# Performance work log

Measured on AMD Instinct MI355X. Metric: run time of the kernel, lower is better.

## Reference

```python
import jax, jax.numpy as jnp
import numpy as np

NEG = -1e9  # additive mask value


def _longformer_attn(x, kv_mask, Wq, bq, Wk, bk, Wv, bv, Wqg, bqg, Wkg, bkg, Wvg, bvg, Wo, bo, H, w, G):
    # x: [B, S, E]; kv_mask: [B, S] (mask*-1 > 0 => global; first G tokens are global by construction)
    B, S, E = x.shape
    D = E // H
    scale = 1.0 / float(D) ** 0.5

    def proj(W, b):  # -> [B, H, S, D]
        return (x @ W + b).reshape(B, S, H, D).transpose(0, 2, 1, 3)

    q = proj(Wq, bq) * scale
    k = proj(Wk, bk)
    v = proj(Wv, bv)

    nc = S // w  # number of query chunks of size w
    # banded keys/values: each chunk of w queries sees a 3w key band (prev/cur/next chunk)
    idx = (jnp.arange(nc) * w)[:, None] + jnp.arange(3 * w)[None, :]  # [nc, 3w] into padded seq

    def band(t):  # [B,H,S,D] -> [B,H,nc,3w,D]
        tp = jnp.pad(t, ((0, 0), (0, 0), (w, w), (0, 0)))
        return tp[:, :, idx, :]

    k3, v3 = band(k), band(v)
    qc = q.reshape(B, H, nc, w, D)
    s_win = jnp.einsum('bhcwd,bhced->bhcwe', qc, k3)  # [B,H,nc,w,3w]

    i = jnp.arange(w)[:, None]
    j = jnp.arange(3 * w)[None, :]
    rel_ok = (j >= i) & (j <= i + 2 * w)  # |key_pos - query_pos| <= w
    keypos = (jnp.arange(nc) * w)[:, None, None] + (jnp.arange(3 * w) - w)[None, None, :]  # [nc,1,3w]
    ok = rel_ok[None] & (keypos >= 0) & (keypos < S) & (keypos >= G)  # global keys handled separately
    s_win = jnp.where(ok[None, None], s_win, NEG)

    # every query also attends to the G global keys (standard projections)
    s_g = jnp.einsum('bhqd,bhgd->bhqg', q, k[:, :, :G])  # [B,H,S,G]
    s_all = jnp.concatenate([s_g, s_win.reshape(B, H, S, 3 * w)], axis=-1)
    p = jax.nn.softmax(s_all, axis=-1)  # joint softmax over global + window keys
    p_g, p_w = p[..., :G], p[..., G:].reshape(B, H, nc, w, 3 * w)

    out = jnp.einsum('bhcwe,bhced->bhcwd', p_w, v3).reshape(B, H, S, D)
    out = out + jnp.einsum('bhqg,bhgd->bhqd', p_g, v[:, :, :G])

    # global query rows: full attention over all tokens with the *global* projections
    qg = (x @ Wqg + bqg).reshape(B, S, H, D).transpose(0, 2, 1, 3)[:, :, :G] * scale
    kg = (x @ Wkg + bkg).reshape(B, S, H, D).transpose(0, 2, 1, 3)
    vg = (x @ Wvg + bvg).reshape(B, S, H, D).transpose(0, 2, 1, 3)
    pg = jax.nn.softmax(jnp.einsum('bhgd,bhsd->bhgs', qg, kg), axis=-1)  # [B,H,G,S]
    out = out.at[:, :, :G].set(jnp.einsum('bhgs,bhsd->bhgd', pg, vg))

    ctx = out.transpose(0, 2, 1, 3).reshape(B, S, E)
    return ctx @ Wo + bo  # wrapper's self.output Linear


def setup_inputs() -> dict:
    key = jax.random.key(0)
    B, S, E, H, w, G = 2, 4096, 1024, 16, 256, 64
    ks = jax.random.split(key, 20)
    x = jax.random.normal(ks[0], (B, S, E), dtype=jnp.float32)
    # key_value_states acts as the mask source: (kv * -1) > 0 marks global tokens
    kv = jnp.zeros((B, S), dtype=jnp.float32).at[:, :G].set(-1.0)

    def lin(k1, k2):
        return (jax.random.normal(k1, (E, E), dtype=jnp.float32) * 0.02,
                jax.random.normal(k2, (E,), dtype=jnp.float32) * 0.02)

    Wq, bq = lin(ks[1], ks[2])
    Wk, bk = lin(ks[3], ks[4])
    Wv, bv = lin(ks[5], ks[6])
    Wqg, bqg = lin(ks[7], ks[8])
    Wkg, bkg = lin(ks[9], ks[10])
    Wvg, bvg = lin(ks[11], ks[12])
    Wo, bo = lin(ks[13], ks[14])
    return {"hidden_states": x, "key_value_states": kv,
            "Wq": Wq, "bq": bq, "Wk": Wk, "bk": bk, "Wv": Wv, "bv": bv,
            "Wqg": Wqg, "bqg": bqg, "Wkg": Wkg, "bkg": bkg, "Wvg": Wvg, "bvg": bvg,
            "Wo": Wo, "bo": bo, "num_heads": H, "window": w, "num_global": G}


def reference(hidden_states, key_value_states, Wq, bq, Wk, bk, Wv, bv, Wqg, bqg, Wkg, bkg, Wvg, bvg, Wo, bo, num_heads, window, num_global):
    return _longformer_attn(hidden_states, key_value_states, Wq, bq, Wk, bk, Wv, bv,
                            Wqg, bqg, Wkg, bkg, Wvg, bvg, Wo, bo,
                            num_heads, window, num_global)
```

## Files before the change

### kernel.cpp

```cpp
#include <hip/hip_runtime.h>

typedef _Float16 half_t;
typedef _Float16 h8 __attribute__((ext_vector_type(8)));
typedef _Float16 h4 __attribute__((ext_vector_type(4)));
typedef float f4 __attribute__((ext_vector_type(4)));

#define DEV __device__ __forceinline__

constexpr int Bc = 2, Sc = 4096, Ec = 1024, Hc = 16, Dc = 64, Wc = 256, Gc = 64;
constexpr float QSCALE = 0.125f;
constexpr float NEGV = -1e9f;

DEV f4 mfma16(h8 a, h8 b, f4 c) {
  return __builtin_amdgcn_mfma_f32_16x16x32_f16(a, b, c, 0, 0, 0);
}

DEV void gl_lds16(const half_t* g, half_t* l) {
  __builtin_amdgcn_global_load_lds((const __attribute__((address_space(1))) void*)g,
                                   (__attribute__((address_space(3))) void*)l, 16, 0, 0);
}


__global__ void cvt_x_kernel(const float* __restrict__ x, half_t* __restrict__ xh) {
  int i = blockIdx.x * 256 + threadIdx.x;
  float4 v = ((const float4*)x)[i];
  h4 o;
  o[0] = (half_t)v.x; o[1] = (half_t)v.y; o[2] = (half_t)v.z; o[3] = (half_t)v.w;
  ((h4*)xh)[i] = o;
}

__global__ void wcvt_kernel(const float* __restrict__ W, half_t* __restrict__ Wt) {
  __shared__ float tile[64][65];
  const int bx = blockIdx.x & 15, by = blockIdx.x >> 4;
  const int tx = threadIdx.x & 63, ty = threadIdx.x >> 6;
  const int n0 = bx * 64, k0 = by * 64;
#pragma unroll
  for (int i = 0; i < 16; ++i) {
    int k = ty + i * 4;
    tile[k][tx] = W[(size_t)(k0 + k) * Ec + n0 + tx];
  }
  __syncthreads();
#pragma unroll
  for (int i = 0; i < 16; ++i) {
    int n = ty + i * 4;
    Wt[(size_t)(n0 + n) * Ec + k0 + tx] = (half_t)tile[tx][n];
  }
}

__global__ __launch_bounds__(256) void gemm_proj(const half_t* __restrict__ A,
                                                 const half_t* __restrict__ Bt,
                                                 const float* __restrict__ bcat,
                                                 half_t* __restrict__ qh, half_t* __restrict__ kh,
                                                 half_t* __restrict__ vt, half_t* __restrict__ kgh,
                                                 half_t* __restrict__ vgt, half_t* __restrict__ qgh) {
  __shared__ __align__(16) half_t Ash[128 * 32];
  __shared__ __align__(16) half_t Bsh[128 * 32];
  const int tid = threadIdx.x;
  const int wv = tid >> 6, lane = tid & 63;
  const int mr = lane & 15, qd = lane >> 4;
  const int wv_m = wv >> 1, wv_n = wv & 1;
  const int col0 = blockIdx.x * 128;
  const int row0 = blockIdx.y * 128;
  const int g = col0 >> 10;

  f4 acc[4][4] = {};

  for (int k0 = 0; k0 < Ec; k0 += 32) {
#pragma unroll
    for (int i = 0; i < 2; ++i) {
      int slot = wv * 128 + i * 64 + lane;
      int r = slot >> 2;
      int kc = (slot & 3) ^ (r & 3);
      gl_lds16(A + (size_t)(row0 + r) * Ec + k0 + kc * 8, Ash + (size_t)(wv * 128 + i * 64) * 8);
      gl_lds16(Bt + (size_t)(col0 + r) * Ec + k0 + kc * 8, Bsh + (size_t)(wv * 128 + i * 64) * 8);
    }
    __syncthreads();
    h8 af[4], bf[4];
#pragma unroll
    for (int mt = 0; mt < 4; ++mt) {
      int r = wv_m * 64 + mt * 16 + mr;
      af[mt] = *(const h8*)(Ash + (size_t)((r << 2) | (qd ^ (r & 3))) * 8);
    }
#pragma unroll
    for (int nt = 0; nt < 4; ++nt) {
      int r = wv_n * 64 + nt * 16 + mr;
      bf[nt] = *(const h8*)(Bsh + (size_t)((r << 2) | (qd ^ (r & 3))) * 8);
    }
#pragma unroll
    for (int mt = 0; mt < 4; ++mt)
#pragma unroll
      for (int nt = 0; nt < 4; ++nt)
        acc[mt][nt] = mfma16(af[mt], bf[nt], acc[mt][nt]);
    __syncthreads();
  }

  const float scale = (g == 0 || g == 5) ? QSCALE : 1.0f;
#pragma unroll
  for (int mt = 0; mt < 4; ++mt) {
#pragma unroll
    for (int nt = 0; nt < 4; ++nt) {
      const int C = col0 + wv_n * 64 + nt * 16 + mr;
      const float bval = bcat[C];
      const int c1 = C & 1023, hh = c1 >> 6, d = c1 & 63;
      const int Rbase = row0 + wv_m * 64 + mt * 16 + qd * 4;
      f4 a = acc[mt][nt];
      if (g == 2 || g == 4) {
        half_t* O = (g == 2) ? vt : vgt;
        int b = Rbase >> 12, s = Rbase & 4095;
        h4 pk;
#pragma unroll
        for (int r = 0; r < 4; ++r) pk[r] = (half_t)(a[r] + bval);
        *(h4*)(O + ((size_t)(b * Hc + hh) * Dc + d) * Sc + s) = pk;
      } else if (g == 5) {
#pragma unroll
        for (int r = 0; r < 4; ++r) {
          int R = Rbase + r;
          int b = R >> 12, s = R & 4095;
          if (s < Gc)
            qgh[((size_t)(b * Hc + hh) * Gc + s) * Dc + d] = (half_t)((a[r] + bval) * scale);
        }
      } else {
        half_t* O = (g == 0) ? qh : (g == 1) ? kh : kgh;
#pragma unroll
        for (int r = 0; r < 4; ++r) {
          int R = Rbase + r;
          int b = R >> 12, s = R & 4095;
          O[((size_t)(b * Hc + hh) * Sc + s) * Dc + d] = (half_t)((a[r] + bval) * scale);
        }
      }
    }
  }
}

__global__ __launch_bounds__(256) void gemm_out(const half_t* __restrict__ A,
                                                const half_t* __restrict__ Bt,
                                                const float* __restrict__ bias,
                                                float* __restrict__ O) {
  __shared__ __align__(16) half_t Ash[128 * 32];
  __shared__ __align__(16) half_t Bsh[128 * 32];
  const int tid = threadIdx.x;
  const int wv = tid >> 6, lane = tid & 63;
  const int mr = lane & 15, qd = lane >> 4;
  const int wv_m = wv >> 1, wv_n = wv & 1;
  const int col0 = blockIdx.x * 128;
  const int row0 = blockIdx.y * 128;

  f4 acc[4][4] = {};

  for (int k0 = 0; k0 < Ec; k0 += 32) {
#pragma unroll
    for (int i = 0; i < 2; ++i) {
      int slot = wv * 128 + i * 64 + lane;
      int r = slot >> 2;
      int kc = (slot & 3) ^ (r & 3);
      gl_lds16(A + (size_t)(row0 + r) * Ec + k0 + kc * 8, Ash + (size_t)(wv * 128 + i * 64) * 8);
      gl_lds16(Bt + (size_t)(col0 + r) * Ec + k0 + kc * 8, Bsh + (size_t)(wv * 128 + i * 64) * 8);
    }
    __syncthreads();
    h8 af[4], bf[4];
#pragma unroll
    for (int mt = 0; mt < 4; ++mt) {
      int r = wv_m * 64 + mt * 16 + mr;
      af[mt] = *(const h8*)(Ash + (size_t)((r << 2) | (qd ^ (r & 3))) * 8);
    }
#pragma unroll
    for (int nt = 0; nt < 4; ++nt) {
      int r = wv_n * 64 + nt * 16 + mr;
      bf[nt] = *(const h8*)(Bsh + (size_t)((r << 2) | (qd ^ (r & 3))) * 8);
    }
#pragma unroll
    for (int mt = 0; mt < 4; ++mt)
#pragma unroll
      for (int nt = 0; nt < 4; ++nt)
        acc[mt][nt] = mfma16(af[mt], bf[nt], acc[mt][nt]);
    __syncthreads();
  }

#pragma unroll
  for (int mt = 0; mt < 4; ++mt) {
#pragma unroll
    for (int nt = 0; nt < 4; ++nt) {
      const int C = col0 + wv_n * 64 + nt * 16 + mr;
      const float bval = bias[C];
      const int Rbase = row0 + wv_m * 64 + mt * 16 + qd * 4;
      f4 a = acc[mt][nt];
#pragma unroll
      for (int r = 0; r < 4; ++r)
        O[(size_t)(Rbase + r) * Ec + C] = a[r] + bval;
    }
  }
}

__global__ __launch_bounds__(256) void win_attn(const half_t* __restrict__ qh,
                                                const half_t* __restrict__ kh,
                                                const half_t* __restrict__ vt,
                                                half_t* __restrict__ ctx) {
  constexpr int PST = 88;
  __shared__ __align__(16) half_t Kb[2][64 * 64];
  __shared__ __align__(16) half_t Vb[2][64 * 64];
  __shared__ __align__(16) half_t Pl[4][16 * PST];
  const int bid = blockIdx.x;
  const int qc = bid & 15, h = (bid >> 4) & 15, b = bid >> 8;
  const int qs = qc << 8;
  const int tid = threadIdx.x, wv = tid >> 6, lane = tid & 63;
  const int mr = lane & 15, qd = lane >> 4;
  const int qw = qs + wv * 64;
  const size_t bh = (size_t)(b * Hc + h);
  const half_t* qb = qh + bh * Sc * Dc;
  const half_t* kb = kh + bh * Sc * Dc;
  const half_t* vb = vt + bh * Dc * Sc;
  half_t* Pw = &Pl[wv][0];

  h8 qf[4][2];
#pragma unroll
  for (int qt = 0; qt < 4; ++qt) {
    const half_t* qrow = qb + (size_t)(qw + qt * 16 + mr) * Dc;
    qf[qt][0] = *(const h8*)(qrow + qd * 8);
    qf[qt][1] = *(const h8*)(qrow + 32 + qd * 8);
  }

  int tiles[14];
  int nT = 0;
  tiles[nT++] = 0;
  {
    int lo = qs - Wc; if (lo < Gc) lo = Gc;
    int hi = qs + 448; if (hi > Sc - 64) hi = Sc - 64;
    for (int kp0 = lo; kp0 <= hi; kp0 += 64) tiles[nT++] = kp0;
  }

  auto stage = [&](int kp0, int bi) {
#pragma unroll
    for (int i = 0; i < 2; ++i) {
      const int seg = wv * 2 + i;
      const int s = seg * 64 + lane;
      const int r = s >> 3;
      const int kc = (s & 7) ^ (r & 7);
      gl_lds16(kb + (size_t)(kp0 + r) * Dc + kc * 8, &Kb[bi][seg * 512]);
      gl_lds16(vb + (size_t)r * Sc + kp0 + kc * 8, &Vb[bi][seg * 512]);
    }
  };

  float m_run[4], l_run[4];
  f4 acc[4][4] = {};
#pragma unroll
  for (int qt = 0; qt < 4; ++qt) { m_run[qt] = -1e30f; l_run[qt] = 0.f; }

  stage(tiles[0], 0);

  for (int t = 0; t < nT; ++t) {
    __syncthreads();
    if (t + 1 < nT) stage(tiles[t + 1], (t + 1) & 1);
    const int kp0 = tiles[t];
    if (t > 0 && (kp0 > qw + 319 || kp0 + 63 < qw - Wc)) continue;

    const half_t* BK = Kb[t & 1];
    const half_t* BV = Vb[t & 1];
    h8 kf[4][2], vf[4][2];
#pragma unroll
    for (int mt = 0; mt < 4; ++mt) {
      const int row = mt * 16 + mr, r7 = row & 7;
      kf[mt][0] = *(const h8*)(BK + (size_t)(row * 8 + (qd ^ r7)) * 8);
      kf[mt][1] = *(const h8*)(BK + (size_t)(row * 8 + ((qd + 4) ^ r7)) * 8);
      vf[mt][0] = *(const h8*)(BV + (size_t)(row * 8 + (qd ^ r7)) * 8);
      vf[mt][1] = *(const h8*)(BV + (size_t)(row * 8 + ((qd + 4) ^ r7)) * 8);
    }
    const bool nomask = (t == 0) || (kp0 >= qw - 193 && kp0 <= qw + 193);

#pragma unroll
    for (int qt = 0; qt < 4; ++qt) {
      f4 sa[4];
#pragma unroll
      for (int mt = 0; mt < 4; ++mt) {
        f4 s = {};
        s = mfma16(kf[mt][0], qf[qt][0], s);
        s = mfma16(kf[mt][1], qf[qt][1], s);
        sa[mt] = s;
      }
      const int q = qw + qt * 16 + mr;
      if (!nomask) {
#pragma unroll
        for (int mt = 0; mt < 4; ++mt)
#pragma unroll
          for (int r = 0; r < 4; ++r) {
            const int kp = kp0 + mt * 16 + qd * 4 + r;
            if (kp < q - Wc || kp > q + Wc) sa[mt][r] = NEGV;
          }
      }
      float tm = -1e30f;
#pragma unroll
      for (int mt = 0; mt < 4; ++mt)
#pragma unroll
        for (int r = 0; r < 4; ++r) tm = fmaxf(tm, sa[mt][r]);
      tm = fmaxf(tm, __shfl_xor(tm, 16));
      tm = fmaxf(tm, __shfl_xor(tm, 32));
      const float mnew = fmaxf(m_run[qt], tm);
      const float alpha = __expf(m_run[qt] - mnew);
      m_run[qt] = mnew;
      float psum = 0.0f;
#pragma unroll
      for (int mt = 0; mt < 4; ++mt) {
        h4 pk;
#pragma unroll
        for (int r = 0; r < 4; ++r) {
          const float p = __expf(sa[mt][r] - mnew);
          psum += p;
          pk[r] = (half_t)p;
        }
        *(h4*)(Pw + mr * PST + mt * 16 + qd * 4) = pk;
      }
      psum += __shfl_xor(psum, 16);
      psum += __shfl_xor(psum, 32);
      l_run[qt] = l_run[qt] * alpha + psum;
#pragma unroll
      for (int mt = 0; mt < 4; ++mt)
#pragma unroll
        for (int r = 0; r < 4; ++r) acc[qt][mt][r] *= alpha;
      const h8 p0 = *(const h8*)(Pw + mr * PST + qd * 8);
      const h8 p1 = *(const h8*)(Pw + mr * PST + 32 + qd * 8);
#pragma unroll
      for (int mt = 0; mt < 4; ++mt) {
        acc[qt][mt] = mfma16(vf[mt][0], p0, acc[qt][mt]);
        acc[qt][mt] = mfma16(vf[mt][1], p1, acc[qt][mt]);
      }
    }
  }

#pragma unroll
  for (int qt = 0; qt < 4; ++qt) {
    const float inv = 1.0f / l_run[qt];
    const int q = qw + qt * 16 + mr;
    half_t* crow = ctx + ((size_t)(b * Sc) + q) * Ec + h * Dc;
#pragma unroll
    for (int mt = 0; mt < 4; ++mt) {
      h4 pk;
#pragma unroll
      for (int r = 0; r < 4; ++r) pk[r] = (half_t)(acc[qt][mt][r] * inv);
      *(h4*)(crow + mt * 16 + qd * 4) = pk;
    }
  }
}


__global__ __launch_bounds__(256) void gq_scores(const half_t* __restrict__ qgh,
                                                 const half_t* __restrict__ kgh,
                                                 float* __restrict__ Sg) {
  const int st = blockIdx.x & 15, h = (blockIdx.x >> 4) & 15, b = blockIdx.x >> 8;
  const int wv = threadIdx.x >> 6, lane = threadIdx.x & 63;
  const int mr = lane & 15, qd = lane >> 4;
  const size_t bh = (size_t)(b * Hc + h);
  const half_t* qb = qgh + bh * Gc * Dc;
  const half_t* kb = kgh + bh * Sc * Dc;
  float* out = Sg + bh * Gc * Sc;

  h8 a0 = *(const h8*)(qb + (size_t)(wv * 16 + mr) * Dc + qd * 8);
  h8 a1 = *(const h8*)(qb + (size_t)(wv * 16 + mr) * Dc + 32 + qd * 8);
#pragma unroll 4
  for (int nt = 0; nt < 16; ++nt) {
    int s = st * 256 + nt * 16 + mr;
    h8 b0 = *(const h8*)(kb + (size_t)s * Dc + qd * 8);
    h8 b1 = *(const h8*)(kb + (size_t)s * Dc + 32 + qd * 8);
    f4 scv = {};
    scv = mfma16(a0, b0, scv);
    scv = mfma16(a1, b1, scv);
#pragma unroll
    for (int r = 0; r < 4; ++r)
      out[(size_t)(wv * 16 + qd * 4 + r) * Sc + st * 256 + nt * 16 + mr] = scv[r];
  }
}

__global__ __launch_bounds__(256) void gq_softmax(const float* __restrict__ Sg,
                                                  half_t* __restrict__ Pg) {
  const int row = blockIdx.x;
  const float* src = Sg + (size_t)row * Sc;
  half_t* dst = Pg + (size_t)row * Sc;
  const int t = threadIdx.x;
  __shared__ float red[4], reds[4];
  float mx = -1e30f;
  for (int i = t; i < Sc; i += 256) mx = fmaxf(mx, src[i]);
#pragma unroll
  for (int o = 1; o < 64; o <<= 1) mx = fmaxf(mx, __shfl_xor(mx, o));
  if ((t & 63) == 0) red[t >> 6] = mx;
  __syncthreads();
  mx = fmaxf(fmaxf(red[0], red[1]), fmaxf(red[2], red[3]));
  float pv[16];
  float sum = 0.f;
  for (int i = t, j = 0; i < Sc; i += 256, ++j) {
    pv[j] = __expf(src[i] - mx);
    sum += pv[j];
  }
#pragma unroll
  for (int o = 1; o < 64; o <<= 1) sum += __shfl_xor(sum, o);
  if ((t & 63) == 0) reds[t >> 6] = sum;
  __syncthreads();
  sum = reds[0] + reds[1] + reds[2] + reds[3];
  float inv = 1.0f / sum;
  for (int i = t, j = 0; i < Sc; i += 256, ++j) dst[i] = (half_t)(pv[j] * inv);
}

__global__ __launch_bounds__(256) void gq_pv(const half_t* __restrict__ Pg,
                                             const half_t* __restrict__ vgt,
                                             half_t* __restrict__ ctx) {
  const int ds = blockIdx.x & 3, h = (blockIdx.x >> 2) & 15, b = blockIdx.x >> 6;
  const int wv = threadIdx.x >> 6, lane = threadIdx.x & 63;
  const int mr = lane & 15, qd = lane >> 4;
  const size_t bh = (size_t)(b * Hc + h);
  const half_t* pb = Pg + bh * Gc * Sc;
  const int d = ds * 16 + mr;
  const half_t* vb = vgt + (bh * Dc + d) * Sc;
  f4 o = {};
  for (int ch = 0; ch < 128; ++ch) {
    h8 af = *(const h8*)(pb + (size_t)(wv * 16 + mr) * Sc + ch * 32 + qd * 8);
    h8 bf = *(const h8*)(vb + ch * 32 + qd * 8);
    o = mfma16(af, bf, o);
  }
#pragma unroll
  for (int r = 0; r < 4; ++r) {
    int g = wv * 16 + qd * 4 + r;
    ctx[(size_t)(b * Sc + g) * Ec + h * Dc + d] = (half_t)o[r];
  }
}


extern "C" void kernel_launch(void* const* d_in, const int* in_sizes, int n_in,
                              void* d_out, int out_size, void* d_ws, size_t ws_size,
                              hipStream_t stream) {
  const float* x   = (const float*)d_in[0];
  const float* Wq  = (const float*)d_in[2];
  const float* bq  = (const float*)d_in[3];
  const float* Wk  = (const float*)d_in[4];
  const float* bk  = (const float*)d_in[5];
  const float* Wv  = (const float*)d_in[6];
  const float* bv  = (const float*)d_in[7];
  const float* Wqg = (const float*)d_in[8];
  const float* bqg = (const float*)d_in[9];
  const float* Wkg = (const float*)d_in[10];
  const float* bkg = (const float*)d_in[11];
  const float* Wvg = (const float*)d_in[12];
  const float* bvg = (const float*)d_in[13];
  const float* Wo  = (const float*)d_in[14];
  const float* bo  = (const float*)d_in[15];
  float* out = (float*)d_out;

  char* ws = (char*)d_ws;
  size_t off = 0;
  auto alloc = [&](size_t bytes) {
    void* p = ws + off;
    off = (off + bytes + 255) & ~(size_t)255;
    return p;
  };
  const size_t BSE2 = (size_t)Bc * Sc * Ec * 2;
  const size_t W2 = (size_t)Ec * Ec * 2;
  half_t* xh   = (half_t*)alloc(BSE2);
  half_t* Wcat = (half_t*)alloc(W2 * 6);
  half_t* WtO  = (half_t*)alloc(W2);
  float*  bcat = (float*)alloc(6 * Ec * 4);
  half_t* qh   = (half_t*)alloc(BSE2);
  half_t* kh   = (half_t*)alloc(BSE2);
  half_t* vt   = (half_t*)alloc(BSE2);
  half_t* kgh  = (half_t*)alloc(BSE2);
  half_t* vgt  = (half_t*)alloc(BSE2);
  half_t* qgh  = (half_t*)alloc((size_t)Bc * Hc * Gc * Dc * 2);
  half_t* ctx  = (half_t*)alloc(BSE2);
  float*  Sg   = (float*)alloc((size_t)Bc * Hc * Gc * Sc * 4);
  half_t* Pg   = (half_t*)alloc((size_t)Bc * Hc * Gc * Sc * 2);
  (void)ws_size; (void)in_sizes; (void)n_in; (void)out_size;

  cvt_x_kernel<<<8192, 256, 0, stream>>>(x, xh);
  wcvt_kernel<<<256, 256, 0, stream>>>(Wq,  Wcat + 0 * Ec * Ec);
  wcvt_kernel<<<256, 256, 0, stream>>>(Wk,  Wcat + 1 * (size_t)Ec * Ec);
  wcvt_kernel<<<256, 256, 0, stream>>>(Wv,  Wcat + 2 * (size_t)Ec * Ec);
  wcvt_kernel<<<256, 256, 0, stream>>>(Wkg, Wcat + 3 * (size_t)Ec * Ec);
  wcvt_kernel<<<256, 256, 0, stream>>>(Wvg, Wcat + 4 * (size_t)Ec * Ec);
  wcvt_kernel<<<256, 256, 0, stream>>>(Wqg, Wcat + 5 * (size_t)Ec * Ec);
  wcvt_kernel<<<256, 256, 0, stream>>>(Wo,  WtO);
  hipMemcpyAsync(bcat + 0 * Ec, bq,  Ec * 4, hipMemcpyDeviceToDevice, stream);
  hipMemcpyAsync(bcat + 1 * Ec, bk,  Ec * 4, hipMemcpyDeviceToDevice, stream);
  hipMemcpyAsync(bcat + 2 * Ec, bv,  Ec * 4, hipMemcpyDeviceToDevice, stream);
  hipMemcpyAsync(bcat + 3 * Ec, bkg, Ec * 4, hipMemcpyDeviceToDevice, stream);
  hipMemcpyAsync(bcat + 4 * Ec, bvg, Ec * 4, hipMemcpyDeviceToDevice, stream);
  hipMemcpyAsync(bcat + 5 * Ec, bqg, Ec * 4, hipMemcpyDeviceToDevice, stream);

  gemm_proj<<<dim3(48, 64), 256, 0, stream>>>(xh, Wcat, bcat, qh, kh, vt, kgh, vgt, qgh);

  win_attn<<<Bc * Hc * (Sc / 256), 256, 0, stream>>>(qh, kh, vt, ctx);

  gq_scores<<<Bc * Hc * 16, 256, 0, stream>>>(qgh, kgh, Sg);
  gq_softmax<<<Bc * Hc * Gc, 256, 0, stream>>>(Sg, Pg);
  gq_pv<<<Bc * Hc * 4, 256, 0, stream>>>(Pg, vgt, ctx);

  gemm_out<<<dim3(8, 64), 256, 0, stream>>>(ctx, WtO, bo, out);
}
```

Before: 486.1 us.

## Fuse prep kernels, skip unused Qg rows, deepen GEMM K-tile, fuse global attention

Merges the x conversion and seven weight-transpose kernels into one launch and drops the bias memcpys by passing the bias pointers directly. The Qg projection now runs only on the 64 global rows of each batch through a dedicated column of 8 blocks instead of the full sequence. Both GEMMs double their K-step to 64 with an 8-way swizzle, halving the number of barriers. The three-kernel global-query path (scores, softmax, PV through global memory) becomes one online-softmax kernel. That kernel launches only 32 blocks, so the global-attention path may be latency-bound.

```diff
diff --git a/kernel.cpp b/kernel.cpp
--- a/kernel.cpp
+++ b/kernel.cpp
@@ -20,20 +20,32 @@
                                    (__attribute__((address_space(3))) void*)l, 16, 0, 0);
 }
 
-
-__global__ void cvt_x_kernel(const float* __restrict__ x, half_t* __restrict__ xh) {
-  int i = blockIdx.x * 256 + threadIdx.x;
-  float4 v = ((const float4*)x)[i];
-  h4 o;
-  o[0] = (half_t)v.x; o[1] = (half_t)v.y; o[2] = (half_t)v.z; o[3] = (half_t)v.w;
-  ((h4*)xh)[i] = o;
-}
-
-__global__ void wcvt_kernel(const float* __restrict__ W, half_t* __restrict__ Wt) {
+__global__ void prep(const float* __restrict__ x,
+                     const float* __restrict__ Wq, const float* __restrict__ Wk,
+                     const float* __restrict__ Wv, const float* __restrict__ Wkg,
+                     const float* __restrict__ Wvg, const float* __restrict__ Wqg,
+                     const float* __restrict__ Wo,
+                     half_t* __restrict__ xh, half_t* __restrict__ Wcat,
+                     half_t* __restrict__ WtO) {
   __shared__ float tile[64][65];
-  const int bx = blockIdx.x & 15, by = blockIdx.x >> 4;
+  const int bx = blockIdx.x;
+  if (bx < 8192) {
+    int i = bx * 256 + threadIdx.x;
+    float4 v = ((const float4*)x)[i];
+    h4 o;
+    o[0] = (half_t)v.x; o[1] = (half_t)v.y; o[2] = (half_t)v.z; o[3] = (half_t)v.w;
+    ((h4*)xh)[i] = o;
+    return;
+  }
+  const int widx = bx - 8192;
+  const int y = widx >> 8;
+  const int xb = widx & 255;
+  const float* W = (y == 0) ? Wq : (y == 1) ? Wk : (y == 2) ? Wv :
+                   (y == 3) ? Wkg : (y == 4) ? Wvg : (y == 5) ? Wqg : Wo;
+  half_t* Wt = (y < 6) ? (Wcat + (size_t)y * Ec * Ec) : WtO;
+  const int bxt = xb & 15, byt = xb >> 4;
   const int tx = threadIdx.x & 63, ty = threadIdx.x >> 6;
-  const int n0 = bx * 64, k0 = by * 64;
+  const int n0 = bxt * 64, k0 = byt * 64;
 #pragma unroll
   for (int i = 0; i < 16; ++i) {
     int k = ty + i * 4;
@@ -49,130 +61,145 @@
 
 __global__ __launch_bounds__(256) void gemm_proj(const half_t* __restrict__ A,
                                                  const half_t* __restrict__ Bt,
-                                                 const float* __restrict__ bcat,
+                                                 const float* __restrict__ bq,
+                                                 const float* __restrict__ bk,
+                                                 const float* __restrict__ bv,
+                                                 const float* __restrict__ bkg,
+                                                 const float* __restrict__ bvg,
+                                                 const float* __restrict__ bqg,
                                                  half_t* __restrict__ qh, half_t* __restrict__ kh,
                                                  half_t* __restrict__ vt, half_t* __restrict__ kgh,
                                                  half_t* __restrict__ vgt, half_t* __restrict__ qgh) {
-  __shared__ __align__(16) half_t Ash[128 * 32];
-  __shared__ __align__(16) half_t Bsh[128 * 32];
+  __shared__ __align__(16) half_t Ash[128 * 64];
+  __shared__ __align__(16) half_t Bsh[128 * 64];
+  const bool qgblk = (blockIdx.x == 40);
+  if (qgblk && blockIdx.y >= 8) return;
+  const int tid = threadIdx.x;
+  const int wv = tid >> 6, lane = tid & 63;
+  const int mr = lane & 15, qd = lane >> 4;
+  const int wv_m = wv >> 1, wv_n = wv & 1;
+  const int col0 = qgblk ? (5 * Ec + (int)blockIdx.y * 128) : (int)blockIdx.x * 128;
+  const int row0 = qgblk ? 0 : (int)blockIdx.y * 128;
+  const int g = col0 >> 10;
+
+  f4 acc[4][4] = {};
+
+  for (int k0 = 0; k0 < Ec; k0 += 64) {
+#pragma unroll
+    for (int i = 0; i < 4; ++i) {
+      int slot = wv * 256 + i * 64 + lane;
+      int r = slot >> 3;
+      int kc = (slot & 7) ^ (r & 7);
+      int ar = qgblk ? ((r < 64) ? r : 4032 + r) : (row0 + r);
+      gl_lds16(A + (size_t)ar * Ec + k0 + kc * 8, Ash + (size_t)(wv * 256 + i * 64) * 8);
+      gl_lds16(Bt + (size_t)(col0 + r) * Ec + k0 + kc * 8, Bsh + (size_t)(wv * 256 + i * 64) * 8);
+    }
+    __syncthreads();
+#pragma unroll
+    for (int u = 0; u < 2; ++u) {
+      h8 af[4], bf[4];
+#pragma unroll
+      for (int mt = 0; mt < 4; ++mt) {
+        int r = wv_m * 64 + mt * 16 + mr;
+        af[mt] = *(const h8*)(Ash + (size_t)(r * 8 + ((qd + u * 4) ^ (r & 7))) * 8);
+      }
+#pragma unroll
+      for (int nt = 0; nt < 4; ++nt) {
+        int r = wv_n * 64 + nt * 16 + mr;
+        bf[nt] = *(const h8*)(Bsh + (size_t)(r * 8 + ((qd + u * 4) ^ (r & 7))) * 8);
+      }
+#pragma unroll
+      for (int mt = 0; mt < 4; ++mt)
+#pragma unroll
+        for (int nt = 0; nt < 4; ++nt)
+          acc[mt][nt] = mfma16(af[mt], bf[nt], acc[mt][nt]);
+    }
+    __syncthreads();
+  }
+
+  const float* bptr = (g == 0) ? bq : (g == 1) ? bk : (g == 2) ? bv :
+                      (g == 3) ? bkg : (g == 4) ? bvg : bqg;
+#pragma unroll
+  for (int mt = 0; mt < 4; ++mt) {
+#pragma unroll
+    for (int nt = 0; nt < 4; ++nt) {
+      const int C = col0 + wv_n * 64 + nt * 16 + mr;
+      const int c1 = C & 1023, hh = c1 >> 6, d = c1 & 63;
+      const float bval = bptr[c1];
+      const int Rbase = row0 + wv_m * 64 + mt * 16 + qd * 4;
+      f4 a = acc[mt][nt];
+      if (g == 2 || g == 4) {
+        half_t* O = (g == 2) ? vt : vgt;
+        int b = Rbase >> 12, s = Rbase & 4095;
+        h4 pk;
+#pragma unroll
+        for (int r = 0; r < 4; ++r) pk[r] = (half_t)(a[r] + bval);
+        *(h4*)(O + ((size_t)(b * Hc + hh) * Dc + d) * Sc + s) = pk;
+      } else if (g == 5) {
+#pragma unroll
+        for (int r = 0; r < 4; ++r) {
+          int rr = Rbase + r;
+          int b = rr >> 6, s = rr & 63;
+          qgh[((size_t)(b * Hc + hh) * Gc + s) * Dc + d] = (half_t)((a[r] + bval) * QSCALE);
+        }
+      } else {
+        half_t* O = (g == 0) ? qh : (g == 1) ? kh : kgh;
+        const float scale = (g == 0) ? QSCALE : 1.0f;
+#pragma unroll
+        for (int r = 0; r < 4; ++r) {
+          int R = Rbase + r;
+          int b = R >> 12, s = R & 4095;
+          O[((size_t)(b * Hc + hh) * Sc + s) * Dc + d] = (half_t)((a[r] + bval) * scale);
+        }
+      }
+    }
+  }
+}
+
+__global__ __launch_bounds__(256) void gemm_out(const half_t* __restrict__ A,
+                                                const half_t* __restrict__ Bt,
+                                                const float* __restrict__ bias,
+                                                float* __restrict__ O) {
+  __shared__ __align__(16) half_t Ash[128 * 64];
+  __shared__ __align__(16) half_t Bsh[128 * 64];
   const int tid = threadIdx.x;
   const int wv = tid >> 6, lane = tid & 63;
   const int mr = lane & 15, qd = lane >> 4;
   const int wv_m = wv >> 1, wv_n = wv & 1;
   const int col0 = blockIdx.x * 128;
   const int row0 = blockIdx.y * 128;
-  const int g = col0 >> 10;
 
   f4 acc[4][4] = {};
 
-  for (int k0 = 0; k0 < Ec; k0 += 32) {
-#pragma unroll
-    for (int i = 0; i < 2; ++i) {
-      int slot = wv * 128 + i * 64 + lane;
-      int r = slot >> 2;
-      int kc = (slot & 3) ^ (r & 3);
-      gl_lds16(A + (size_t)(row0 + r) * Ec + k0 + kc * 8, Ash + (size_t)(wv * 128 + i * 64) * 8);
-      gl_lds16(Bt + (size_t)(col0 + r) * Ec + k0 + kc * 8, Bsh + (size_t)(wv * 128 + i * 64) * 8);
+  for (int k0 = 0; k0 < Ec; k0 += 64) {
+#pragma unroll
+    for (int i = 0; i < 4; ++i) {
+      int slot = wv * 256 + i * 64 + lane;
+      int r = slot >> 3;
+      int kc = (slot & 7) ^ (r & 7);
+      gl_lds16(A + (size_t)(row0 + r) * Ec + k0 + kc * 8, Ash + (size_t)(wv * 256 + i * 64) * 8);
+      gl_lds16(Bt + (size_t)(col0 + r) * Ec + k0 + kc * 8, Bsh + (size_t)(wv * 256 + i * 64) * 8);
     }
     __syncthreads();
-    h8 af[4], bf[4];
-#pragma unroll
-    for (int mt = 0; mt < 4; ++mt) {
-      int r = wv_m * 64 + mt * 16 + mr;
-      af[mt] = *(const h8*)(Ash + (size_t)((r << 2) | (qd ^ (r & 3))) * 8);
-    }
-#pragma unroll
-    for (int nt = 0; nt < 4; ++nt) {
-      int r = wv_n * 64 + nt * 16 + mr;
-      bf[nt] = *(const h8*)(Bsh + (size_t)((r << 2) | (qd ^ (r & 3))) * 8);
-    }
-#pragma unroll
-    for (int mt = 0; mt < 4; ++mt)
-#pragma unroll
-      for (int nt = 0; nt < 4; ++nt)
-        acc[mt][nt] = mfma16(af[mt], bf[nt], acc[mt][nt]);
-    __syncthreads();
-  }
-
-  const float scale = (g == 0 || g == 5) ? QSCALE : 1.0f;
-#pragma unroll
-  for (int mt = 0; mt < 4; ++mt) {
-#pragma unroll
-    for (int nt = 0; nt < 4; ++nt) {
-      const int C = col0 + wv_n * 64 + nt * 16 + mr;
-      const float bval = bcat[C];
-      const int c1 = C & 1023, hh = c1 >> 6, d = c1 & 63;
-      const int Rbase = row0 + wv_m * 64 + mt * 16 + qd * 4;
-      f4 a = acc[mt][nt];
-      if (g == 2 || g == 4) {
-        half_t* O = (g == 2) ? vt : vgt;
-        int b = Rbase >> 12, s = Rbase & 4095;
-        h4 pk;
-#pragma unroll
-        for (int r = 0; r < 4; ++r) pk[r] = (half_t)(a[r] + bval);
-        *(h4*)(O + ((size_t)(b * Hc + hh) * Dc + d) * Sc + s) = pk;
-      } else if (g == 5) {
-#pragma unroll
-        for (int r = 0; r < 4; ++r) {
-          int R = Rbase + r;
-          int b = R >> 12, s = R & 4095;
-          if (s < Gc)
-            qgh[((size_t)(b * Hc + hh) * Gc + s) * Dc + d] = (half_t)((a[r] + bval) * scale);
-        }
-      } else {
-        half_t* O = (g == 0) ? qh : (g == 1) ? kh : kgh;
-#pragma unroll
-        for (int r = 0; r < 4; ++r) {
-          int R = Rbase + r;
-          int b = R >> 12, s = R & 4095;
-          O[((size_t)(b * Hc + hh) * Sc + s) * Dc + d] = (half_t)((a[r] + bval) * scale);
-        }
-      }
-    }
-  }
-}
-
-__global__ __launch_bounds__(256) void gemm_out(const half_t* __restrict__ A,
-                                                const half_t* __restrict__ Bt,
-                                                const float* __restrict__ bias,
-                                                float* __restrict__ O) {
-  __shared__ __align__(16) half_t Ash[128 * 32];
-  __shared__ __align__(16) half_t Bsh[128 * 32];
-  const int tid = threadIdx.x;
-  const int wv = tid >> 6, lane = tid & 63;
-  const int mr = lane & 15, qd = lane >> 4;
-  const int wv_m = wv >> 1, wv_n = wv & 1;
-  const int col0 = blockIdx.x * 128;
-  const int row0 = blockIdx.y * 128;
-
-  f4 acc[4][4] = {};
-
-  for (int k0 = 0; k0 < Ec; k0 += 32) {
-#pragma unroll
-    for (int i = 0; i < 2; ++i) {
-      int slot = wv * 128 + i * 64 + lane;
-      int r = slot >> 2;
-      int kc = (slot & 3) ^ (r & 3);
-      gl_lds16(A + (size_t)(row0 + r) * Ec + k0 + kc * 8, Ash + (size_t)(wv * 128 + i * 64) * 8);
-      gl_lds16(Bt + (size_t)(col0 + r) * Ec + k0 + kc * 8, Bsh + (size_t)(wv * 128 + i * 64) * 8);
-    }
-    __syncthreads();
-    h8 af[4], bf[4];
-#pragma unroll
-    for (int mt = 0; mt < 4; ++mt) {
-      int r = wv_m * 64 + mt * 16 + mr;
-      af[mt] = *(const h8*)(Ash + (size_t)((r << 2) | (qd ^ (r & 3))) * 8);
-    }
-#pragma unroll
-    for (int nt = 0; nt < 4; ++nt) {
-      int r = wv_n * 64 + nt * 16 + mr;
-      bf[nt] = *(const h8*)(Bsh + (size_t)((r << 2) | (qd ^ (r & 3))) * 8);
-    }
-#pragma unroll
-    for (int mt = 0; mt < 4; ++mt)
-#pragma unroll
-      for (int nt = 0; nt < 4; ++nt)
-        acc[mt][nt] = mfma16(af[mt], bf[nt], acc[mt][nt]);
+#pragma unroll
+    for (int u = 0; u < 2; ++u) {
+      h8 af[4], bf[4];
+#pragma unroll
+      for (int mt = 0; mt < 4; ++mt) {
+        int r = wv_m * 64 + mt * 16 + mr;
+        af[mt] = *(const h8*)(Ash + (size_t)(r * 8 + ((qd + u * 4) ^ (r & 7))) * 8);
+      }
+#pragma unroll
+      for (int nt = 0; nt < 4; ++nt) {
+        int r = wv_n * 64 + nt * 16 + mr;
+        bf[nt] = *(const h8*)(Bsh + (size_t)(r * 8 + ((qd + u * 4) ^ (r & 7))) * 8);
+      }
+#pragma unroll
+      for (int mt = 0; mt < 4; ++mt)
+#pragma unroll
+        for (int nt = 0; nt < 4; ++nt)
+          acc[mt][nt] = mfma16(af[mt], bf[nt], acc[mt][nt]);
+    }
     __syncthreads();
   }
 
@@ -340,83 +367,90 @@
   }
 }
 
-
-__global__ __launch_bounds__(256) void gq_scores(const half_t* __restrict__ qgh,
-                                                 const half_t* __restrict__ kgh,
-                                                 float* __restrict__ Sg) {
-  const int st = blockIdx.x & 15, h = (blockIdx.x >> 4) & 15, b = blockIdx.x >> 8;
-  const int wv = threadIdx.x >> 6, lane = threadIdx.x & 63;
+__global__ __launch_bounds__(256) void gq_fused(const half_t* __restrict__ qgh,
+                                                const half_t* __restrict__ kgh,
+                                                const half_t* __restrict__ vgt,
+                                                half_t* __restrict__ ctx) {
+  constexpr int PST = 88;
+  __shared__ __align__(16) half_t Pl[4][16 * PST];
+  const int h = blockIdx.x & 15, b = blockIdx.x >> 4;
+  const int tid = threadIdx.x, wv = tid >> 6, lane = tid & 63;
   const int mr = lane & 15, qd = lane >> 4;
   const size_t bh = (size_t)(b * Hc + h);
   const half_t* qb = qgh + bh * Gc * Dc;
   const half_t* kb = kgh + bh * Sc * Dc;
-  float* out = Sg + bh * Gc * Sc;
-
-  h8 a0 = *(const h8*)(qb + (size_t)(wv * 16 + mr) * Dc + qd * 8);
-  h8 a1 = *(const h8*)(qb + (size_t)(wv * 16 + mr) * Dc + 32 + qd * 8);
-#pragma unroll 4
-  for (int nt = 0; nt < 16; ++nt) {
-    int s = st * 256 + nt * 16 + mr;
-    h8 b0 = *(const h8*)(kb + (size_t)s * Dc + qd * 8);
-    h8 b1 = *(const h8*)(kb + (size_t)s * Dc + 32 + qd * 8);
-    f4 scv = {};
-    scv = mfma16(a0, b0, scv);
-    scv = mfma16(a1, b1, scv);
-#pragma unroll
-    for (int r = 0; r < 4; ++r)
-      out[(size_t)(wv * 16 + qd * 4 + r) * Sc + st * 256 + nt * 16 + mr] = scv[r];
-  }
-}
-
-__global__ __launch_bounds__(256) void gq_softmax(const float* __restrict__ Sg,
-                                                  half_t* __restrict__ Pg) {
-  const int row = blockIdx.x;
-  const float* src = Sg + (size_t)row * Sc;
-  half_t* dst = Pg + (size_t)row * Sc;
-  const int t = threadIdx.x;
-  __shared__ float red[4], reds[4];
-  float mx = -1e30f;
-  for (int i = t; i < Sc; i += 256) mx = fmaxf(mx, src[i]);
-#pragma unroll
-  for (int o = 1; o < 64; o <<= 1) mx = fmaxf(mx, __shfl_xor(mx, o));
-  if ((t & 63) == 0) red[t >> 6] = mx;
-  __syncthreads();
-  mx = fmaxf(fmaxf(red[0], red[1]), fmaxf(red[2], red[3]));
-  float pv[16];
-  float sum = 0.f;
-  for (int i = t, j = 0; i < Sc; i += 256, ++j) {
-    pv[j] = __expf(src[i] - mx);
-    sum += pv[j];
-  }
-#pragma unroll
-  for (int o = 1; o < 64; o <<= 1) sum += __shfl_xor(sum, o);
-  if ((t & 63) == 0) reds[t >> 6] = sum;
-  __syncthreads();
-  sum = reds[0] + reds[1] + reds[2] + reds[3];
-  float inv = 1.0f / sum;
-  for (int i = t, j = 0; i < Sc; i += 256, ++j) dst[i] = (half_t)(pv[j] * inv);
-}
-
-__global__ __launch_bounds__(256) void gq_pv(const half_t* __restrict__ Pg,
-                                             const half_t* __restrict__ vgt,
-                                             half_t* __restrict__ ctx) {
-  const int ds = blockIdx.x & 3, h = (blockIdx.x >> 2) & 15, b = blockIdx.x >> 6;
-  const int wv = threadIdx.x >> 6, lane = threadIdx.x & 63;
-  const int mr = lane & 15, qd = lane >> 4;
-  const size_t bh = (size_t)(b * Hc + h);
-  const half_t* pb = Pg + bh * Gc * Sc;
-  const int d = ds * 16 + mr;
-  const half_t* vb = vgt + (bh * Dc + d) * Sc;
-  f4 o = {};
-  for (int ch = 0; ch < 128; ++ch) {
-    h8 af = *(const h8*)(pb + (size_t)(wv * 16 + mr) * Sc + ch * 32 + qd * 8);
-    h8 bf = *(const h8*)(vb + ch * 32 + qd * 8);
-    o = mfma16(af, bf, o);
-  }
-#pragma unroll
-  for (int r = 0; r < 4; ++r) {
-    int g = wv * 16 + qd * 4 + r;
-    ctx[(size_t)(b * Sc + g) * Ec + h * Dc + d] = (half_t)o[r];
+  const half_t* vb = vgt + bh * Dc * Sc;
+  half_t* Pw = &Pl[wv][0];
+
+  const int qrow = wv * 16 + mr;
+  const h8 qf0 = *(const h8*)(qb + (size_t)qrow * Dc + qd * 8);
+  const h8 qf1 = *(const h8*)(qb + (size_t)qrow * Dc + 32 + qd * 8);
+
+  float m_run = -1e30f, l_run = 0.f;
+  f4 acc[4] = {};
+
+  for (int t = 0; t < 64; ++t) {
+    const int kp0 = t * 64;
+    f4 sa[4];
+#pragma unroll
+    for (int mt = 0; mt < 4; ++mt) {
+      const int kp = kp0 + mt * 16 + mr;
+      h8 kf0 = *(const h8*)(kb + (size_t)kp * Dc + qd * 8);
+      h8 kf1 = *(const h8*)(kb + (size_t)kp * Dc + 32 + qd * 8);
+      f4 s = {};
+      s = mfma16(kf0, qf0, s);
+      s = mfma16(kf1, qf1, s);
+      sa[mt] = s;
+    }
+    float tm = -1e30f;
+#pragma unroll
+    for (int mt = 0; mt < 4; ++mt)
+#pragma unroll
+      for (int r = 0; r < 4; ++r) tm = fmaxf(tm, sa[mt][r]);
+    tm = fmaxf(tm, __shfl_xor(tm, 16));
+    tm = fmaxf(tm, __shfl_xor(tm, 32));
+    const float mnew = fmaxf(m_run, tm);
+    const float alpha = __expf(m_run - mnew);
+    m_run = mnew;
+    float psum = 0.0f;
+#pragma unroll
+    for (int mt = 0; mt < 4; ++mt) {
+      h4 pk;
+#pragma unroll
+      for (int r = 0; r < 4; ++r) {
+        const float p = __expf(sa[mt][r] - mnew);
+        psum += p;
+        pk[r] = (half_t)p;
+      }
+      *(h4*)(Pw + mr * PST + mt * 16 + qd * 4) = pk;
+    }
+    psum += __shfl_xor(psum, 16);
+    psum += __shfl_xor(psum, 32);
+    l_run = l_run * alpha + psum;
+#pragma unroll
+    for (int mt = 0; mt < 4; ++mt)
+#pragma unroll
+      for (int r = 0; r < 4; ++r) acc[mt][r] *= alpha;
+    const h8 p0 = *(const h8*)(Pw + mr * PST + qd * 8);
+    const h8 p1 = *(const h8*)(Pw + mr * PST + 32 + qd * 8);
+#pragma unroll
+    for (int mt = 0; mt < 4; ++mt) {
+      const h8 vf0 = *(const h8*)(vb + (size_t)(mt * 16 + mr) * Sc + kp0 + qd * 8);
+      const h8 vf1 = *(const h8*)(vb + (size_t)(mt * 16 + mr) * Sc + kp0 + 32 + qd * 8);
+      acc[mt] = mfma16(vf0, p0, acc[mt]);
+      acc[mt] = mfma16(vf1, p1, acc[mt]);
+    }
+  }
+
+  const float inv = 1.0f / l_run;
+  const int g = wv * 16 + mr;
+  half_t* crow = ctx + ((size_t)(b * Sc) + g) * Ec + h * Dc;
+#pragma unroll
+  for (int mt = 0; mt < 4; ++mt) {
+    h4 pk;
+#pragma unroll
+    for (int r = 0; r < 4; ++r) pk[r] = (half_t)(acc[mt][r] * inv);
+    *(h4*)(crow + mt * 16 + qd * 4) = pk;
   }
 }
 
@@ -453,7 +487,6 @@
   half_t* xh   = (half_t*)alloc(BSE2);
   half_t* Wcat = (half_t*)alloc(W2 * 6);
   half_t* WtO  = (half_t*)alloc(W2);
-  float*  bcat = (float*)alloc(6 * Ec * 4);
   half_t* qh   = (half_t*)alloc(BSE2);
   half_t* kh   = (half_t*)alloc(BSE2);
   half_t* vt   = (half_t*)alloc(BSE2);
@@ -461,32 +494,17 @@
   half_t* vgt  = (half_t*)alloc(BSE2);
   half_t* qgh  = (half_t*)alloc((size_t)Bc * Hc * Gc * Dc * 2);
   half_t* ctx  = (half_t*)alloc(BSE2);
-  float*  Sg   = (float*)alloc((size_t)Bc * Hc * Gc * Sc * 4);
-  half_t* Pg   = (half_t*)alloc((size_t)Bc * Hc * Gc * Sc * 2);
   (void)ws_size; (void)in_sizes; (void)n_in; (void)out_size;
 
-  cvt_x_kernel<<<8192, 256, 0, stream>>>(x, xh);
-  wcvt_kernel<<<256, 256, 0, stream>>>(Wq,  Wcat + 0 * Ec * Ec);
-  wcvt_kernel<<<256, 256, 0, stream>>>(Wk,  Wcat + 1 * (size_t)Ec * Ec);
-  wcvt_kernel<<<256, 256, 0, stream>>>(Wv,  Wcat + 2 * (size_t)Ec * Ec);
-  wcvt_kernel<<<256, 256, 0, stream>>>(Wkg, Wcat + 3 * (size_t)Ec * Ec);
-  wcvt_kernel<<<256, 256, 0, stream>>>(Wvg, Wcat + 4 * (size_t)Ec * Ec);
-  wcvt_kernel<<<256, 256, 0, stream>>>(Wqg, Wcat + 5 * (size_t)Ec * Ec);
-  wcvt_kernel<<<256, 256, 0, stream>>>(Wo,  WtO);
-  hipMemcpyAsync(bcat + 0 * Ec, bq,  Ec * 4, hipMemcpyDeviceToDevice, stream);
-  hipMemcpyAsync(bcat + 1 * Ec, bk,  Ec * 4, hipMemcpyDeviceToDevice, stream);
-  hipMemcpyAsync(bcat + 2 * Ec, bv,  Ec * 4, hipMemcpyDeviceToDevice, stream);
-  hipMemcpyAsync(bcat + 3 * Ec, bkg, Ec * 4, hipMemcpyDeviceToDevice, stream);
-  hipMemcpyAsync(bcat + 4 * Ec, bvg, Ec * 4, hipMemcpyDeviceToDevice, stream);
-  hipMemcpyAsync(bcat + 5 * Ec, bqg, Ec * 4, hipMemcpyDeviceToDevice, stream);
-
-  gemm_proj<<<dim3(48, 64), 256, 0, stream>>>(xh, Wcat, bcat, qh, kh, vt, kgh, vgt, qgh);
+  prep<<<8192 + 7 * 256, 256, 0, stream>>>(x, Wq, Wk, Wv, Wkg, Wvg, Wqg, Wo,
+                                           xh, Wcat, WtO);
+
+  gemm_proj<<<dim3(41, 64), 256, 0, stream>>>(xh, Wcat, bq, bk, bv, bkg, bvg, bqg,
+                                              qh, kh, vt, kgh, vgt, qgh);
 
   win_attn<<<Bc * Hc * (Sc / 256), 256, 0, stream>>>(qh, kh, vt, ctx);
 
-  gq_scores<<<Bc * Hc * 16, 256, 0, stream>>>(qgh, kgh, Sg);
-  gq_softmax<<<Bc * Hc * Gc, 256, 0, stream>>>(Sg, Pg);
-  gq_pv<<<Bc * Hc * 4, 256, 0, stream>>>(Pg, vgt, ctx);
+  gq_fused<<<Bc * Hc, 256, 0, stream>>>(qgh, kgh, vgt, ctx);
 
   gemm_out<<<dim3(8, 64), 256, 0, stream>>>(ctx, WtO, bo, out);
 }
```

New measurement: 505.5 us. 4.0% more time.
